# Kernel optimization log

Measured on AMD Instinct MI355X. Metric: run time of the kernel, lower is better.

Reference implementation:

```python
import jax, jax.numpy as jnp
import numpy as np

L = 2          # lags
D = 64         # latent_size
H = 128        # hidden_dim
NB = 3         # num_layers == n_blocks
B, T = 256, 1024


def setup_inputs() -> dict:
    key = jax.random.key(0)
    ks = jax.random.split(key, 20)
    sd = 0.1
    inp = {
        'x': jax.random.normal(ks[0], (B, T, D), jnp.float32),
        # f1: 3 hidden Linear(L*D=128 -> 128), all same shape so stacked, then out Linear(128 -> 64)
        'f1_hW': jax.random.normal(ks[1], (NB, H, H), jnp.float32) * sd,
        'f1_hb': jax.random.normal(ks[2], (NB, H), jnp.float32) * sd,
        'f1_oW': jax.random.normal(ks[3], (D, H), jnp.float32) * sd,
        'f1_ob': jax.random.normal(ks[4], (D,), jnp.float32) * sd,
        # flow: per block, s_net and t_net each Lin(D,H), Lin(H,H), Lin(H,D) (torch y = x@W.T + b)
        'sW0': jax.random.normal(ks[5], (NB, H, D), jnp.float32) * sd,
        'sb0': jax.random.normal(ks[6], (NB, H), jnp.float32) * sd,
        'sW1': jax.random.normal(ks[7], (NB, H, H), jnp.float32) * sd,
        'sb1': jax.random.normal(ks[8], (NB, H), jnp.float32) * sd,
        'sW2': jax.random.normal(ks[9], (NB, D, H), jnp.float32) * sd,
        'sb2': jax.random.normal(ks[10], (NB, D), jnp.float32) * sd,
        'tW0': jax.random.normal(ks[11], (NB, H, D), jnp.float32) * sd,
        'tb0': jax.random.normal(ks[12], (NB, H), jnp.float32) * sd,
        'tW1': jax.random.normal(ks[13], (NB, H, H), jnp.float32) * sd,
        'tb1': jax.random.normal(ks[14], (NB, H), jnp.float32) * sd,
        'tW2': jax.random.normal(ks[15], (NB, D, H), jnp.float32) * sd,
        'tb2': jax.random.normal(ks[16], (NB, D), jnp.float32) * sd,
    }
    return inp


def _leaky(z):
    return jnp.where(z >= 0, z, 0.2 * z)  # leap's NLayerLeakyMLP uses LeakyReLU(0.2)


def _flow(xt, sW0, sb0, sW1, sb1, sW2, sb2, tW0, tb0, tW1, tb1, tW2, tb2):
    # RealNVP-style affine coupling stack, no batch norm. xt: (N, D)
    m = (jnp.arange(D) % 2).astype(xt.dtype)  # alternating mask, flips per block
    u = xt
    logdet = jnp.zeros((xt.shape[0],), xt.dtype)
    for i in range(NB):
        mx = u * m
        s = jnp.tanh(mx @ sW0[i].T + sb0[i])
        s = jnp.tanh(s @ sW1[i].T + sb1[i])
        s = s @ sW2[i].T + sb2[i]
        t = jax.nn.relu(mx @ tW0[i].T + tb0[i])
        t = jax.nn.relu(t @ tW1[i].T + tb1[i])
        t = t @ tW2[i].T + tb2[i]
        u = mx + (1.0 - m) * (u - t) * jnp.exp(-s)
        logdet = logdet + jnp.sum(-(1.0 - m) * s, axis=1)
        m = 1.0 - m
    return u, logdet


def reference(x, f1_hW, f1_hb, f1_oW, f1_ob, sW0, sb0, sW1, sb1, sW2, sb2,
              tW0, tb0, tW1, tb1, tW2, tb2):
    Bs, Ts, Din = x.shape
    # f2 inverse flow on x[:, L:, :] flattened to (B*(T-L), D)
    xt = x[:, L:, :].reshape(-1, Din)
    x_inv, logdet = _flow(xt, sW0, sb0, sW1, sb1, sW2, sb2,
                          tW0, tb0, tW1, tb1, tW2, tb2)
    x_inv = x_inv.reshape(Bs, Ts - L, Din)
    # vectorized sliding-window MLP (replaces the per-timestep python loop)
    idx = jnp.arange(Ts - L)[:, None] + jnp.arange(L)        # (T-L, L)
    win = x[:, idx, :].reshape(Bs, Ts - L, L * Din)          # (B, T-L, L*D)
    h = win
    for i in range(NB):
        h = _leaky(h @ f1_hW[i].T + f1_hb[i])
    residuals = h @ f1_oW.T + f1_ob - x_inv                  # (B, T-L, D)
    log_abs_det_jacobian = jnp.sum(logdet.reshape(Bs, Ts - L), axis=1)  # (B,)
    return residuals, log_abs_det_jacobian
```

## Files before the change

kernel.cpp:

```cpp
#include <hip/hip_runtime.h>

#define DEV __device__ __forceinline__

typedef __attribute__((ext_vector_type(8)))  short bf16x8;
typedef __attribute__((ext_vector_type(4)))  short s16x4;
typedef __attribute__((ext_vector_type(4)))  float f32x4;
typedef __attribute__((ext_vector_type(16))) float f32x16;
typedef __attribute__((ext_vector_type(4)))  unsigned u32x4;

constexpr int Tt = 1024, TLr = 1022;
constexpr long WSW_BYTES = 704512;

#define MFMA32(a,b,c) __builtin_amdgcn_mfma_f32_32x32x16_bf16((a),(b),(c),0,0,0)

#define GLDS16(gp, lp) __builtin_amdgcn_global_load_lds( \
    (__attribute__((address_space(1))) void*)(void*)(gp), \
    (__attribute__((address_space(3))) void*)(void*)(lp), 16, 0, 0)

DEV short bf16hi(float f){
  unsigned u = __builtin_bit_cast(unsigned, f);
  u += 0x7FFFu + ((u >> 16) & 1u);
  return (short)(u >> 16);
}
DEV float bf2f(short h){
  unsigned u = ((unsigned)(unsigned short)h) << 16;
  return __builtin_bit_cast(float, u);
}
DEV void splitbf(float f, short &h, short &l){
  h = bf16hi(f);
  l = bf16hi(f - bf2f(h));
}

DEV unsigned cvtpk(float a, float b){
  unsigned r;
  asm("v_cvt_pk_bf16_f32 %0, %1, %2" : "=v"(r) : "v"(a), "v"(b));
  return r;
}
DEV void plswap(unsigned &a, unsigned &b){
  auto r = __builtin_amdgcn_permlane32_swap((int)a, (int)b, false, false);
  a = (unsigned)r[0]; b = (unsigned)r[1];
}

template<int A> DEV float actf(float x){
  if constexpr (A == 1){
    float e = __expf(2.f * x);
    return 1.f - 2.f * __builtin_amdgcn_rcpf(e + 1.f);
  } else if constexpr (A == 2){
    return fmaxf(x, 0.f);
  } else if constexpr (A == 3){
    return x >= 0.f ? x : 0.2f * x;
  }
  return x;
}

template<int BYTES>
DEV void pref(const char* __restrict__ wsW, long off, char* dst, int tid){
  #pragma unroll
  for (int it = 0; it < BYTES / 4096; ++it)
    GLDS16(wsW + off + it * 4096 + tid * 16, dst + it * 4096 + tid * 16);
}

DEV void packTile(const f32x16& c, unsigned (&Bg0)[4], unsigned (&Bg1)[4]){
  unsigned p0 = cvtpk(c[0], c[1]),  p1 = cvtpk(c[2], c[3]);
  unsigned p2 = cvtpk(c[4], c[5]),  p3 = cvtpk(c[6], c[7]);
  plswap(p0, p2); plswap(p1, p3);
  Bg0[0] = p0; Bg0[1] = p1; Bg0[2] = p2; Bg0[3] = p3;
  p0 = cvtpk(c[8],  c[9]);  p1 = cvtpk(c[10], c[11]);
  p2 = cvtpk(c[12], c[13]); p3 = cvtpk(c[14], c[15]);
  plswap(p0, p2); plswap(p1, p3);
  Bg1[0] = p0; Bg1[1] = p1; Bg1[2] = p2; Bg1[3] = p3;
}

template<int KT,int G,int GI,int MOUT,bool LO,int ACT,int MODE>
DEV void computeMT(const char* __restrict__ Ws, const float* __restrict__ bias,
                   const unsigned (&Bin)[2][8][4], unsigned (&Bout)[2][8][4],
                   f32x16 (&uA)[2][2], float (&ldet)[2],
                   float* __restrict__ residBase, int keep, int rowW,
                   int lane, int h4)
{
  constexpr int BS = LO ? 2048 : 1024;
  f32x16 acc[2];
  #pragma unroll
  for (int q = 0; q < 4; ++q){
    f32x4 bv = *(const f32x4*)(bias + 32 * MOUT + 8 * q + h4);
    #pragma unroll
    for (int j = 0; j < 4; ++j){ acc[0][4*q+j] = bv[j]; acc[1][4*q+j] = bv[j]; }
  }
  #pragma unroll
  for (int kt = 0; kt < KT; ++kt){
    const char* wp = Ws + (kt * G + GI) * BS + lane * 16;
    bf16x8 Ah = *(const bf16x8*)wp;
    #pragma unroll
    for (int n = 0; n < 2; ++n){
      u32x4 bw = {Bin[n][kt][0], Bin[n][kt][1], Bin[n][kt][2], Bin[n][kt][3]};
      acc[n] = MFMA32(Ah, __builtin_bit_cast(bf16x8, bw), acc[n]);
    }
    if constexpr (LO){
      bf16x8 Al = *(const bf16x8*)(wp + 1024);
      #pragma unroll
      for (int n = 0; n < 2; ++n){
        u32x4 bw = {Bin[n][kt][0], Bin[n][kt][1], Bin[n][kt][2], Bin[n][kt][3]};
        acc[n] = MFMA32(Al, __builtin_bit_cast(bf16x8, bw), acc[n]);
      }
    }
  }
  if constexpr (MODE == 0){
    #pragma unroll
    for (int n = 0; n < 2; ++n){
      #pragma unroll
      for (int i = 0; i < 16; ++i) acc[n][i] = actf<ACT>(acc[n][i]);
      packTile(acc[n], Bout[n][2 * MOUT], Bout[n][2 * MOUT + 1]);
    }
  } else if constexpr (MODE == 1){
    #pragma unroll
    for (int n = 0; n < 2; ++n)
      #pragma unroll
      for (int r = 0; r < 16; ++r)
        if ((r & 1) != keep) uA[MOUT][n][r] -= acc[n][r];
  } else if constexpr (MODE == 2){
    #pragma unroll
    for (int n = 0; n < 2; ++n)
      #pragma unroll
      for (int r = 0; r < 16; ++r)
        if ((r & 1) != keep){
          uA[MOUT][n][r] *= __expf(-acc[n][r]);
          ldet[n] -= acc[n][r];
        }
  } else {
    const int col = lane & 31;
    #pragma unroll
    for (int n = 0; n < 2; ++n){
      const int tau = rowW + n * 32 + col;
      if (tau < TLr){
        float* rp = residBase + (long)tau * 64 + 32 * MOUT + h4;
        #pragma unroll
        for (int q = 0; q < 4; ++q){
          f32x4 st;
          #pragma unroll
          for (int j = 0; j < 4; ++j)
            st[j] = acc[n][4 * q + j] - uA[MOUT][n][4 * q + j];
          *(f32x4*)(rp + 8 * q) = st;
        }
      }
    }
  }
}

DEV void buildMaskedB(const f32x16 (&u)[2][2], unsigned (&B)[2][8][4], int keep){
  const float mOdd  = (keep == 1) ? 1.f : 0.f;
  const float mEven = 1.f - mOdd;
  #pragma unroll
  for (int n = 0; n < 2; ++n)
    #pragma unroll
    for (int mi = 0; mi < 2; ++mi){
      f32x16 v;
      #pragma unroll
      for (int r = 0; r < 16; ++r)
        v[r] = u[mi][n][r] * ((r & 1) ? mOdd : mEven);
      packTile(v, B[n][2 * mi], B[n][2 * mi + 1]);
    }
}

DEV void buildWin(unsigned (&B)[2][8][4], const float* __restrict__ xb,
                  int rowW, int lane){
  const int col = lane & 31, h = lane >> 5;
  #pragma unroll
  for (int n = 0; n < 2; ++n){
    const int tau = rowW + n * 32 + col;
    #pragma unroll
    for (int g = 0; g < 8; ++g){
      int xr = tau + (g >= 4 ? 1 : 0);
      if (xr > Tt - 1) xr = Tt - 1;
      const int fo = (16 * g + 8 * h) & 63;
      const float* p = xb + xr * 64 + fo;
      f32x4 a = *(const f32x4*)p, b = *(const f32x4*)(p + 4);
      B[n][g][0] = cvtpk(a[0], a[1]); B[n][g][1] = cvtpk(a[2], a[3]);
      B[n][g][2] = cvtpk(b[0], b[1]); B[n][g][3] = cvtpk(b[2], b[3]);
    }
  }
}

__global__ void pnl_conv(const float* __restrict__ sW0, const float* __restrict__ sW1,
                         const float* __restrict__ sW2, const float* __restrict__ tW0,
                         const float* __restrict__ tW1, const float* __restrict__ tW2,
                         const float* __restrict__ f1_hW, const float* __restrict__ f1_oW,
                         char* __restrict__ wsW)
{
  const int cid = blockIdx.x * 256 + threadIdx.x;
  const float* src; long base; int hs, unit, BS, lg; bool LO;
  if (cid < 24576){
    const int blk = cid >> 13, r = cid & 8191;
    const long bb = (long)blk * 196608;
    if      (r < 1024){ src = tW0 + blk*8192;  hs=6; base=bb;        BS=1024; lg=2; LO=false; unit=r; }
    else if (r < 3072){ src = tW1 + blk*16384; hs=7; base=bb+16384;  BS=1024; lg=1; LO=false; unit=r-1024; }
    else if (r < 4096){ src = tW2 + blk*8192;  hs=7; base=bb+49152;  BS=1024; lg=1; LO=false; unit=r-3072; }
    else if (r < 5120){ src = sW0 + blk*8192;  hs=6; base=bb+65536;  BS=2048; lg=1; LO=true;  unit=r-4096; }
    else if (r < 7168){ src = sW1 + blk*16384; hs=7; base=bb+98304;  BS=2048; lg=0; LO=true;  unit=r-5120; }
    else              { src = sW2 + blk*8192;  hs=7; base=bb+163840; BS=2048; lg=0; LO=true;  unit=r-7168; }
  } else {
    const int r = cid - 24576;
    if (r < 6144){ const int l = r >> 11; src = f1_hW + l*16384; hs=7; base=589824+(long)l*32768; BS=1024; lg=1; LO=false; unit=r&2047; }
    else         { src = f1_oW; hs=7; base=688128; BS=1024; lg=1; LO=false; unit=r-6144; }
  }
  const int e    = unit << 3;
  const int feat = e >> hs;
  const int k    = e & ((1 << hs) - 1);
  const int m    = feat >> 5;
  const int stage = m >> lg;
  const int gi    = m & ((1 << lg) - 1);
  const int lane  = (feat & 31) | (((k >> 3) & 1) << 5);
  const long off  = base + (long)stage * 16384
                  + (long)((((k >> 4) << lg) + gi) * BS) + lane * 16;
  const float* sp = src + ((long)feat << hs) + k;
  f32x4 v0 = *(const f32x4*)sp, v1 = *(const f32x4*)(sp + 4);
  s16x4 ha, hb, la, lb;
  #pragma unroll
  for (int j = 0; j < 4; ++j){
    short hh, ll;
    splitbf(v0[j], hh, ll); ha[j] = hh; la[j] = ll;
    splitbf(v1[j], hh, ll); hb[j] = hh; lb[j] = ll;
  }
  *(s16x4*)(wsW + off)     = ha;
  *(s16x4*)(wsW + off + 8) = hb;
  if (LO){
    *(s16x4*)(wsW + off + 1024)     = la;
    *(s16x4*)(wsW + off + 1024 + 8) = lb;
  }
}

#define CMT(KT,G,GI,MOUT,LO,ACT,MODE,WS,BIAS,BIN,BOUT) \
  computeMT<KT,G,GI,MOUT,LO,ACT,MODE>(WS,BIAS,BIN,BOUT,uA,ldet,residBase,keep,rowW,lane,h4)

__global__ __launch_bounds__(256, 2)
void pnl_main(const float* __restrict__ x,
              const float* __restrict__ f1_hb, const float* __restrict__ f1_ob,
              const float* __restrict__ sb0, const float* __restrict__ sb1,
              const float* __restrict__ sb2, const float* __restrict__ tb0,
              const float* __restrict__ tb1, const float* __restrict__ tb2,
              const char* __restrict__ wsW,
              float* __restrict__ resid, float* __restrict__ wsPart)
{
  __shared__ __align__(16) char Wb[2][16384];

  const int tid  = threadIdx.x, w = tid >> 6, lane = tid & 63;
  const int col  = lane & 31, h4 = (lane >> 5) * 4;
  const int bIdx = blockIdx.x >> 2;
  const int t0w  = (blockIdx.x & 3) << 8;
  const int rowW = t0w + w * 64;
  const float* xb = x + (long)bIdx * Tt * 64;
  float* __restrict__ residBase = resid + (long)bIdx * TLr * 64;

  pref<16384>(wsW, 0, Wb[0], tid);

  f32x16 uA[2][2];
  #pragma unroll
  for (int mi = 0; mi < 2; ++mi)
    #pragma unroll
    for (int n = 0; n < 2; ++n){
      int xr = rowW + n * 32 + col + 2; if (xr > Tt - 1) xr = Tt - 1;
      #pragma unroll
      for (int q = 0; q < 4; ++q){
        f32x4 v = *(const f32x4*)(xb + xr * 64 + 32 * mi + 8 * q + h4);
        #pragma unroll
        for (int j = 0; j < 4; ++j) uA[mi][n][4 * q + j] = v[j];
      }
    }

  float ldet[2] = {0.f, 0.f};
  unsigned Bx[2][8][4], By[2][8][4];

  buildMaskedB(uA, Bx, 1);
  __syncthreads();

  #pragma unroll 1
  for (int blk = 0; blk < 3; ++blk){
    const long bb = (long)blk * 196608;
    const int keep = 1 - (blk & 1);
    const float* tb0b = tb0 + blk * 128; const float* tb1b = tb1 + blk * 128;
    const float* tb2b = tb2 + blk * 64;
    const float* sb0b = sb0 + blk * 128; const float* sb1b = sb1 + blk * 128;
    const float* sb2b = sb2 + blk * 64;

    pref<16384>(wsW, bb + 16384, Wb[1], tid);
    CMT(4,4,0,0,false,2,0, Wb[0], tb0b, Bx, By);
    CMT(4,4,1,1,false,2,0, Wb[0], tb0b, Bx, By);
    CMT(4,4,2,2,false,2,0, Wb[0], tb0b, Bx, By);
    CMT(4,4,3,3,false,2,0, Wb[0], tb0b, Bx, By);
    __syncthreads();
    pref<16384>(wsW, bb + 32768, Wb[0], tid);
    CMT(8,2,0,0,false,2,0, Wb[1], tb1b, By, Bx);
    CMT(8,2,1,1,false,2,0, Wb[1], tb1b, By, Bx);
    __syncthreads();
    pref<16384>(wsW, bb + 49152, Wb[1], tid);
    CMT(8,2,0,2,false,2,0, Wb[0], tb1b, By, Bx);
    CMT(8,2,1,3,false,2,0, Wb[0], tb1b, By, Bx);
    __syncthreads();
    pref<16384>(wsW, bb + 65536, Wb[0], tid);
    CMT(8,2,0,0,false,0,1, Wb[1], tb2b, Bx, By);
    CMT(8,2,1,1,false,0,1, Wb[1], tb2b, Bx, By);
    buildMaskedB(uA, By, keep);
    __syncthreads();
    pref<16384>(wsW, bb + 81920, Wb[1], tid);
    CMT(4,2,0,0,true,1,0, Wb[0], sb0b, By, Bx);
    CMT(4,2,1,1,true,1,0, Wb[0], sb0b, By, Bx);
    __syncthreads();
    pref<16384>(wsW, bb + 98304, Wb[0], tid);
    CMT(4,2,0,2,true,1,0, Wb[1], sb0b, By, Bx);
    CMT(4,2,1,3,true,1,0, Wb[1], sb0b, By, Bx);
    __syncthreads();
    pref<16384>(wsW, bb + 114688, Wb[1], tid);
    CMT(8,1,0,0,true,1,0, Wb[0], sb1b, Bx, By);
    __syncthreads();
    pref<16384>(wsW, bb + 131072, Wb[0], tid);
    CMT(8,1,0,1,true,1,0, Wb[1], sb1b, Bx, By);
    __syncthreads();
    pref<16384>(wsW, bb + 147456, Wb[1], tid);
    CMT(8,1,0,2,true,1,0, Wb[0], sb1b, Bx, By);
    __syncthreads();
    pref<16384>(wsW, bb + 163840, Wb[0], tid);
    CMT(8,1,0,3,true,1,0, Wb[1], sb1b, Bx, By);
    __syncthreads();
    pref<16384>(wsW, bb + 180224, Wb[1], tid);
    CMT(8,1,0,0,true,0,2, Wb[0], sb2b, By, Bx);
    __syncthreads();
    if (blk < 2) pref<16384>(wsW, bb + 196608, Wb[0], tid);
    else         pref<16384>(wsW, 589824,      Wb[0], tid);
    CMT(8,1,0,1,true,0,2, Wb[1], sb2b, By, Bx);
    if (blk < 2) buildMaskedB(uA, Bx, 1 - ((blk + 1) & 1));
    else         buildWin(Bx, xb, rowW, lane);
    __syncthreads();
  }

  {
    const int keep = 0;
    const float* tbD = f1_hb;
    (void)tbD;
    pref<16384>(wsW, 606208, Wb[1], tid);
    CMT(8,2,0,0,false,3,0, Wb[0], f1_hb, Bx, By);
    CMT(8,2,1,1,false,3,0, Wb[0], f1_hb, Bx, By);
    __syncthreads();
    pref<16384>(wsW, 622592, Wb[0], tid);
    CMT(8,2,0,2,false,3,0, Wb[1], f1_hb, Bx, By);
    CMT(8,2,1,3,false,3,0, Wb[1], f1_hb, Bx, By);
    __syncthreads();
    pref<16384>(wsW, 638976, Wb[1], tid);
    CMT(8,2,0,0,false,3,0, Wb[0], f1_hb + 128, By, Bx);
    CMT(8,2,1,1,false,3,0, Wb[0], f1_hb + 128, By, Bx);
    __syncthreads();
    pref<16384>(wsW, 655360, Wb[0], tid);
    CMT(8,2,0,2,false,3,0, Wb[1], f1_hb + 128, By, Bx);
    CMT(8,2,1,3,false,3,0, Wb[1], f1_hb + 128, By, Bx);
    __syncthreads();
    pref<16384>(wsW, 671744, Wb[1], tid);
    CMT(8,2,0,0,false,3,0, Wb[0], f1_hb + 256, Bx, By);
    CMT(8,2,1,1,false,3,0, Wb[0], f1_hb + 256, Bx, By);
    __syncthreads();
    pref<16384>(wsW, 688128, Wb[0], tid);
    CMT(8,2,0,2,false,3,0, Wb[1], f1_hb + 256, Bx, By);
    CMT(8,2,1,3,false,3,0, Wb[1], f1_hb + 256, Bx, By);
    __syncthreads();
    CMT(8,2,0,0,false,0,3, Wb[0], f1_ob, By, Bx);
    CMT(8,2,1,1,false,0,3, Wb[0], f1_ob, By, Bx);
  }

  const int tau0 = rowW + col, tau1 = rowW + 32 + col;
  float s = (tau0 < TLr ? ldet[0] : 0.f) + (tau1 < TLr ? ldet[1] : 0.f);
  #pragma unroll
  for (int off = 1; off < 64; off <<= 1) s += __shfl_xor(s, off);
  if (lane == 0) wsPart[blockIdx.x * 4 + w] = s;
}

__global__ void pnl_ldet(const float* __restrict__ ws, float* __restrict__ outLd){
  const int b = threadIdx.x;
  float s = 0.f;
  #pragma unroll
  for (int t = 0; t < 16; ++t) s += ws[b * 16 + t];
  outLd[b] = s;
}

extern "C" void kernel_launch(void* const* d_in, const int* in_sizes, int n_in,
                              void* d_out, int out_size, void* d_ws, size_t ws_size,
                              hipStream_t stream){
  const float* x     = (const float*)d_in[0];
  const float* f1_hW = (const float*)d_in[1];
  const float* f1_hb = (const float*)d_in[2];
  const float* f1_oW = (const float*)d_in[3];
  const float* f1_ob = (const float*)d_in[4];
  const float* sW0   = (const float*)d_in[5];
  const float* sb0   = (const float*)d_in[6];
  const float* sW1   = (const float*)d_in[7];
  const float* sb1   = (const float*)d_in[8];
  const float* sW2   = (const float*)d_in[9];
  const float* sb2   = (const float*)d_in[10];
  const float* tW0   = (const float*)d_in[11];
  const float* tb0   = (const float*)d_in[12];
  const float* tW1   = (const float*)d_in[13];
  const float* tb1   = (const float*)d_in[14];
  const float* tW2   = (const float*)d_in[15];
  const float* tb2   = (const float*)d_in[16];

  char*  wsW    = (char*)d_ws;
  float* wsPart = (float*)(wsW + WSW_BYTES);
  float* resid  = (float*)d_out;
  float* outLd  = resid + (long)256 * TLr * 64;

  pnl_conv<<<dim3(124), dim3(256), 0, stream>>>(sW0, sW1, sW2, tW0, tW1, tW2,
                                                f1_hW, f1_oW, wsW);
  pnl_main<<<dim3(1024), dim3(256), 0, stream>>>(
      x, f1_hb, f1_ob, sb0, sb1, sb2, tb0, tb1, tb2, wsW, resid, wsPart);
  pnl_ldet<<<dim3(1), dim3(256), 0, stream>>>(wsPart, outLd);
}
```

Baseline: 232.3 us.

## Triple-buffer weight stages in LDS with vmcnt-based waits and single barriers

Result: slower. 248.3 us (+6.9%).

```diff
diff --git a/kernel.cpp b/kernel.cpp
--- a/kernel.cpp
+++ b/kernel.cpp
@@ -16,6 +16,11 @@
 #define GLDS16(gp, lp) __builtin_amdgcn_global_load_lds( \
     (__attribute__((address_space(1))) void*)(void*)(gp), \
     (__attribute__((address_space(3))) void*)(void*)(lp), 16, 0, 0)
+
+#define WAITV4() asm volatile("s_waitcnt vmcnt(4)" ::: "memory")
+#define WAITV0() asm volatile("s_waitcnt vmcnt(0)" ::: "memory")
+#define BARX()   do { __builtin_amdgcn_s_barrier(); \
+                      __builtin_amdgcn_sched_barrier(0); } while(0)
 
 DEV short bf16hi(float f){
   unsigned u = __builtin_bit_cast(unsigned, f);
@@ -53,11 +58,11 @@
   return x;
 }
 
-template<int BYTES>
-DEV void pref(const char* __restrict__ wsW, long off, char* dst, int tid){
-  #pragma unroll
-  for (int it = 0; it < BYTES / 4096; ++it)
-    GLDS16(wsW + off + it * 4096 + tid * 16, dst + it * 4096 + tid * 16);
+DEV void prefStage(const char* __restrict__ wsW, long k, char* dst, int tid){
+  const char* s = wsW + (k << 14);
+  #pragma unroll
+  for (int it = 0; it < 4; ++it)
+    GLDS16(s + it * 4096 + tid * 16, dst + it * 4096 + tid * 16);
 }
 
 DEV void packTile(const f32x16& c, unsigned (&Bg0)[4], unsigned (&Bg1)[4]){
@@ -240,7 +245,10 @@
               const char* __restrict__ wsW,
               float* __restrict__ resid, float* __restrict__ wsPart)
 {
-  __shared__ __align__(16) char Wb[2][16384];
+  __shared__ __align__(16) char Wb[49152];
+  char* const W0 = Wb;
+  char* const W1 = Wb + 16384;
+  char* const W2 = Wb + 32768;
 
   const int tid  = threadIdx.x, w = tid >> 6, lane = tid & 63;
   const int col  = lane & 31, h4 = (lane >> 5) * 4;
@@ -250,8 +258,6 @@
   const float* xb = x + (long)bIdx * Tt * 64;
   float* __restrict__ residBase = resid + (long)bIdx * TLr * 64;
 
-  pref<16384>(wsW, 0, Wb[0], tid);
-
   f32x16 uA[2][2];
   #pragma unroll
   for (int mi = 0; mi < 2; ++mi)
@@ -265,102 +271,85 @@
         for (int j = 0; j < 4; ++j) uA[mi][n][4 * q + j] = v[j];
       }
     }
+  __builtin_amdgcn_sched_barrier(0);
+
+  prefStage(wsW, 0, W0, tid);
+  prefStage(wsW, 1, W1, tid);
 
   float ldet[2] = {0.f, 0.f};
   unsigned Bx[2][8][4], By[2][8][4];
 
   buildMaskedB(uA, Bx, 1);
-  __syncthreads();
 
   #pragma unroll 1
   for (int blk = 0; blk < 3; ++blk){
-    const long bb = (long)blk * 196608;
+    const long kb = (long)blk * 12;
     const int keep = 1 - (blk & 1);
     const float* tb0b = tb0 + blk * 128; const float* tb1b = tb1 + blk * 128;
     const float* tb2b = tb2 + blk * 64;
     const float* sb0b = sb0 + blk * 128; const float* sb1b = sb1 + blk * 128;
     const float* sb2b = sb2 + blk * 64;
 
-    pref<16384>(wsW, bb + 16384, Wb[1], tid);
-    CMT(4,4,0,0,false,2,0, Wb[0], tb0b, Bx, By);
-    CMT(4,4,1,1,false,2,0, Wb[0], tb0b, Bx, By);
-    CMT(4,4,2,2,false,2,0, Wb[0], tb0b, Bx, By);
-    CMT(4,4,3,3,false,2,0, Wb[0], tb0b, Bx, By);
-    __syncthreads();
-    pref<16384>(wsW, bb + 32768, Wb[0], tid);
-    CMT(8,2,0,0,false,2,0, Wb[1], tb1b, By, Bx);
-    CMT(8,2,1,1,false,2,0, Wb[1], tb1b, By, Bx);
-    __syncthreads();
-    pref<16384>(wsW, bb + 49152, Wb[1], tid);
-    CMT(8,2,0,2,false,2,0, Wb[0], tb1b, By, Bx);
-    CMT(8,2,1,3,false,2,0, Wb[0], tb1b, By, Bx);
-    __syncthreads();
-    pref<16384>(wsW, bb + 65536, Wb[0], tid);
-    CMT(8,2,0,0,false,0,1, Wb[1], tb2b, Bx, By);
-    CMT(8,2,1,1,false,0,1, Wb[1], tb2b, Bx, By);
+    WAITV4(); BARX(); prefStage(wsW, kb + 2, W2, tid);
+    CMT(4,4,0,0,false,2,0, W0, tb0b, Bx, By);
+    CMT(4,4,1,1,false,2,0, W0, tb0b, Bx, By);
+    CMT(4,4,2,2,false,2,0, W0, tb0b, Bx, By);
+    CMT(4,4,3,3,false,2,0, W0, tb0b, Bx, By);
+    WAITV4(); BARX(); prefStage(wsW, kb + 3, W0, tid);
+    CMT(8,2,0,0,false,2,0, W1, tb1b, By, Bx);
+    CMT(8,2,1,1,false,2,0, W1, tb1b, By, Bx);
+    WAITV4(); BARX(); prefStage(wsW, kb + 4, W1, tid);
+    CMT(8,2,0,2,false,2,0, W2, tb1b, By, Bx);
+    CMT(8,2,1,3,false,2,0, W2, tb1b, By, Bx);
+    WAITV4(); BARX(); prefStage(wsW, kb + 5, W2, tid);
+    CMT(8,2,0,0,false,0,1, W0, tb2b, Bx, By);
+    CMT(8,2,1,1,false,0,1, W0, tb2b, Bx, By);
     buildMaskedB(uA, By, keep);
-    __syncthreads();
-    pref<16384>(wsW, bb + 81920, Wb[1], tid);
-    CMT(4,2,0,0,true,1,0, Wb[0], sb0b, By, Bx);
-    CMT(4,2,1,1,true,1,0, Wb[0], sb0b, By, Bx);
-    __syncthreads();
-    pref<16384>(wsW, bb + 98304, Wb[0], tid);
-    CMT(4,2,0,2,true,1,0, Wb[1], sb0b, By, Bx);
-    CMT(4,2,1,3,true,1,0, Wb[1], sb0b, By, Bx);
-    __syncthreads();
-    pref<16384>(wsW, bb + 114688, Wb[1], tid);
-    CMT(8,1,0,0,true,1,0, Wb[0], sb1b, Bx, By);
-    __syncthreads();
-    pref<16384>(wsW, bb + 131072, Wb[0], tid);
-    CMT(8,1,0,1,true,1,0, Wb[1], sb1b, Bx, By);
-    __syncthreads();
-    pref<16384>(wsW, bb + 147456, Wb[1], tid);
-    CMT(8,1,0,2,true,1,0, Wb[0], sb1b, Bx, By);
-    __syncthreads();
-    pref<16384>(wsW, bb + 163840, Wb[0], tid);
-    CMT(8,1,0,3,true,1,0, Wb[1], sb1b, Bx, By);
-    __syncthreads();
-    pref<16384>(wsW, bb + 180224, Wb[1], tid);
-    CMT(8,1,0,0,true,0,2, Wb[0], sb2b, By, Bx);
-    __syncthreads();
-    if (blk < 2) pref<16384>(wsW, bb + 196608, Wb[0], tid);
-    else         pref<16384>(wsW, 589824,      Wb[0], tid);
-    CMT(8,1,0,1,true,0,2, Wb[1], sb2b, By, Bx);
+    WAITV4(); BARX(); prefStage(wsW, kb + 6, W0, tid);
+    CMT(4,2,0,0,true,1,0, W1, sb0b, By, Bx);
+    CMT(4,2,1,1,true,1,0, W1, sb0b, By, Bx);
+    WAITV4(); BARX(); prefStage(wsW, kb + 7, W1, tid);
+    CMT(4,2,0,2,true,1,0, W2, sb0b, By, Bx);
+    CMT(4,2,1,3,true,1,0, W2, sb0b, By, Bx);
+    WAITV4(); BARX(); prefStage(wsW, kb + 8, W2, tid);
+    CMT(8,1,0,0,true,1,0, W0, sb1b, Bx, By);
+    WAITV4(); BARX(); prefStage(wsW, kb + 9, W0, tid);
+    CMT(8,1,0,1,true,1,0, W1, sb1b, Bx, By);
+    WAITV4(); BARX(); prefStage(wsW, kb + 10, W1, tid);
+    CMT(8,1,0,2,true,1,0, W2, sb1b, Bx, By);
+    WAITV4(); BARX(); prefStage(wsW, kb + 11, W2, tid);
+    CMT(8,1,0,3,true,1,0, W0, sb1b, Bx, By);
+    WAITV4(); BARX(); prefStage(wsW, kb + 12, W0, tid);
+    CMT(8,1,0,0,true,0,2, W1, sb2b, By, Bx);
+    WAITV4(); BARX(); prefStage(wsW, kb + 13, W1, tid);
+    CMT(8,1,0,1,true,0,2, W2, sb2b, By, Bx);
     if (blk < 2) buildMaskedB(uA, Bx, 1 - ((blk + 1) & 1));
     else         buildWin(Bx, xb, rowW, lane);
-    __syncthreads();
   }
 
   {
     const int keep = 0;
-    const float* tbD = f1_hb;
-    (void)tbD;
-    pref<16384>(wsW, 606208, Wb[1], tid);
-    CMT(8,2,0,0,false,3,0, Wb[0], f1_hb, Bx, By);
-    CMT(8,2,1,1,false,3,0, Wb[0], f1_hb, Bx, By);
-    __syncthreads();
-    pref<16384>(wsW, 622592, Wb[0], tid);
-    CMT(8,2,0,2,false,3,0, Wb[1], f1_hb, Bx, By);
-    CMT(8,2,1,3,false,3,0, Wb[1], f1_hb, Bx, By);
-    __syncthreads();
-    pref<16384>(wsW, 638976, Wb[1], tid);
-    CMT(8,2,0,0,false,3,0, Wb[0], f1_hb + 128, By, Bx);
-    CMT(8,2,1,1,false,3,0, Wb[0], f1_hb + 128, By, Bx);
-    __syncthreads();
-    pref<16384>(wsW, 655360, Wb[0], tid);
-    CMT(8,2,0,2,false,3,0, Wb[1], f1_hb + 128, By, Bx);
-    CMT(8,2,1,3,false,3,0, Wb[1], f1_hb + 128, By, Bx);
-    __syncthreads();
-    pref<16384>(wsW, 671744, Wb[1], tid);
-    CMT(8,2,0,0,false,3,0, Wb[0], f1_hb + 256, Bx, By);
-    CMT(8,2,1,1,false,3,0, Wb[0], f1_hb + 256, Bx, By);
-    __syncthreads();
-    pref<16384>(wsW, 688128, Wb[0], tid);
-    CMT(8,2,0,2,false,3,0, Wb[1], f1_hb + 256, Bx, By);
-    CMT(8,2,1,3,false,3,0, Wb[1], f1_hb + 256, Bx, By);
-    __syncthreads();
-    CMT(8,2,0,0,false,0,3, Wb[0], f1_ob, By, Bx);
-    CMT(8,2,1,1,false,0,3, Wb[0], f1_ob, By, Bx);
+    WAITV4(); BARX(); prefStage(wsW, 38, W2, tid);
+    CMT(8,2,0,0,false,3,0, W0, f1_hb, Bx, By);
+    CMT(8,2,1,1,false,3,0, W0, f1_hb, Bx, By);
+    WAITV4(); BARX(); prefStage(wsW, 39, W0, tid);
+    CMT(8,2,0,2,false,3,0, W1, f1_hb, Bx, By);
+    CMT(8,2,1,3,false,3,0, W1, f1_hb, Bx, By);
+    WAITV4(); BARX(); prefStage(wsW, 40, W1, tid);
+    CMT(8,2,0,0,false,3,0, W2, f1_hb + 128, By, Bx);
+    CMT(8,2,1,1,false,3,0, W2, f1_hb + 128, By, Bx);
+    WAITV4(); BARX(); prefStage(wsW, 41, W2, tid);
+    CMT(8,2,0,2,false,3,0, W0, f1_hb + 128, By, Bx);
+    CMT(8,2,1,3,false,3,0, W0, f1_hb + 128, By, Bx);
+    WAITV4(); BARX(); prefStage(wsW, 42, W0, tid);
+    CMT(8,2,0,0,false,3,0, W1, f1_hb + 256, Bx, By);
+    CMT(8,2,1,1,false,3,0, W1, f1_hb + 256, Bx, By);
+    WAITV4(); BARX();
+    CMT(8,2,0,2,false,3,0, W2, f1_hb + 256, Bx, By);
+    CMT(8,2,1,3,false,3,0, W2, f1_hb + 256, Bx, By);
+    WAITV0(); BARX();
+    CMT(8,2,0,0,false,0,3, W0, f1_ob, By, Bx);
+    CMT(8,2,1,1,false,0,3, W0, f1_ob, By, Bx);
   }
 
   const int tau0 = rowW + col, tau1 = rowW + 32 + col;
```

## Drop bf16 hi/lo split for s-net first two layers and add MFMA priority

Applied to the files above, without the earlier changes.

Result: faster. 199.8 us, median of 2 (-14.0%).

```diff
diff --git a/kernel.cpp b/kernel.cpp
--- a/kernel.cpp
+++ b/kernel.cpp
@@ -9,7 +9,7 @@
 typedef __attribute__((ext_vector_type(4)))  unsigned u32x4;
 
 constexpr int Tt = 1024, TLr = 1022;
-constexpr long WSW_BYTES = 704512;
+constexpr long WSW_BYTES = 557056;
 
 #define MFMA32(a,b,c) __builtin_amdgcn_mfma_f32_32x32x16_bf16((a),(b),(c),0,0,0)
 
@@ -53,11 +53,11 @@
   return x;
 }
 
-template<int BYTES>
-DEV void pref(const char* __restrict__ wsW, long off, char* dst, int tid){
-  #pragma unroll
-  for (int it = 0; it < BYTES / 4096; ++it)
-    GLDS16(wsW + off + it * 4096 + tid * 16, dst + it * 4096 + tid * 16);
+DEV void prefStage(const char* __restrict__ wsW, long k, char* dst, int tid){
+  const char* s = wsW + (k << 14);
+  #pragma unroll
+  for (int it = 0; it < 4; ++it)
+    GLDS16(s + it * 4096 + tid * 16, dst + it * 4096 + tid * 16);
 }
 
 DEV void packTile(const f32x16& c, unsigned (&Bg0)[4], unsigned (&Bg1)[4]){
@@ -86,6 +86,7 @@
     #pragma unroll
     for (int j = 0; j < 4; ++j){ acc[0][4*q+j] = bv[j]; acc[1][4*q+j] = bv[j]; }
   }
+  __builtin_amdgcn_s_setprio(1);
   #pragma unroll
   for (int kt = 0; kt < KT; ++kt){
     const char* wp = Ws + (kt * G + GI) * BS + lane * 16;
@@ -104,6 +105,7 @@
       }
     }
   }
+  __builtin_amdgcn_s_setprio(0);
   if constexpr (MODE == 0){
     #pragma unroll
     for (int n = 0; n < 2; ++n){
@@ -190,17 +192,17 @@
   const float* src; long base; int hs, unit, BS, lg; bool LO;
   if (cid < 24576){
     const int blk = cid >> 13, r = cid & 8191;
-    const long bb = (long)blk * 196608;
+    const long bb = (long)blk * 147456;
     if      (r < 1024){ src = tW0 + blk*8192;  hs=6; base=bb;        BS=1024; lg=2; LO=false; unit=r; }
     else if (r < 3072){ src = tW1 + blk*16384; hs=7; base=bb+16384;  BS=1024; lg=1; LO=false; unit=r-1024; }
     else if (r < 4096){ src = tW2 + blk*8192;  hs=7; base=bb+49152;  BS=1024; lg=1; LO=false; unit=r-3072; }
-    else if (r < 5120){ src = sW0 + blk*8192;  hs=6; base=bb+65536;  BS=2048; lg=1; LO=true;  unit=r-4096; }
-    else if (r < 7168){ src = sW1 + blk*16384; hs=7; base=bb+98304;  BS=2048; lg=0; LO=true;  unit=r-5120; }
-    else              { src = sW2 + blk*8192;  hs=7; base=bb+163840; BS=2048; lg=0; LO=true;  unit=r-7168; }
+    else if (r < 5120){ src = sW0 + blk*8192;  hs=6; base=bb+65536;  BS=1024; lg=2; LO=false; unit=r-4096; }
+    else if (r < 7168){ src = sW1 + blk*16384; hs=7; base=bb+81920;  BS=1024; lg=1; LO=false; unit=r-5120; }
+    else              { src = sW2 + blk*8192;  hs=7; base=bb+114688; BS=2048; lg=0; LO=true;  unit=r-7168; }
   } else {
     const int r = cid - 24576;
-    if (r < 6144){ const int l = r >> 11; src = f1_hW + l*16384; hs=7; base=589824+(long)l*32768; BS=1024; lg=1; LO=false; unit=r&2047; }
-    else         { src = f1_oW; hs=7; base=688128; BS=1024; lg=1; LO=false; unit=r-6144; }
+    if (r < 6144){ const int l = r >> 11; src = f1_hW + l*16384; hs=7; base=442368+(long)l*32768; BS=1024; lg=1; LO=false; unit=r&2047; }
+    else         { src = f1_oW; hs=7; base=540672; BS=1024; lg=1; LO=false; unit=r-6144; }
   }
   const int e    = unit << 3;
   const int feat = e >> hs;
@@ -250,7 +252,7 @@
   const float* xb = x + (long)bIdx * Tt * 64;
   float* __restrict__ residBase = resid + (long)bIdx * TLr * 64;
 
-  pref<16384>(wsW, 0, Wb[0], tid);
+  prefStage(wsW, 0, Wb[0], tid);
 
   f32x16 uA[2][2];
   #pragma unroll
@@ -274,58 +276,54 @@
 
   #pragma unroll 1
   for (int blk = 0; blk < 3; ++blk){
-    const long bb = (long)blk * 196608;
+    const int kb = blk * 9;
+    const int par = kb & 1;
+    char* const WA = Wb[par];
+    char* const WB = Wb[par ^ 1];
     const int keep = 1 - (blk & 1);
     const float* tb0b = tb0 + blk * 128; const float* tb1b = tb1 + blk * 128;
     const float* tb2b = tb2 + blk * 64;
     const float* sb0b = sb0 + blk * 128; const float* sb1b = sb1 + blk * 128;
     const float* sb2b = sb2 + blk * 64;
 
-    pref<16384>(wsW, bb + 16384, Wb[1], tid);
-    CMT(4,4,0,0,false,2,0, Wb[0], tb0b, Bx, By);
-    CMT(4,4,1,1,false,2,0, Wb[0], tb0b, Bx, By);
-    CMT(4,4,2,2,false,2,0, Wb[0], tb0b, Bx, By);
-    CMT(4,4,3,3,false,2,0, Wb[0], tb0b, Bx, By);
-    __syncthreads();
-    pref<16384>(wsW, bb + 32768, Wb[0], tid);
-    CMT(8,2,0,0,false,2,0, Wb[1], tb1b, By, Bx);
-    CMT(8,2,1,1,false,2,0, Wb[1], tb1b, By, Bx);
-    __syncthreads();
-    pref<16384>(wsW, bb + 49152, Wb[1], tid);
-    CMT(8,2,0,2,false,2,0, Wb[0], tb1b, By, Bx);
-    CMT(8,2,1,3,false,2,0, Wb[0], tb1b, By, Bx);
-    __syncthreads();
-    pref<16384>(wsW, bb + 65536, Wb[0], tid);
-    CMT(8,2,0,0,false,0,1, Wb[1], tb2b, Bx, By);
-    CMT(8,2,1,1,false,0,1, Wb[1], tb2b, Bx, By);
+    prefStage(wsW, kb + 1, WB, tid);
+    CMT(4,4,0,0,false,2,0, WA, tb0b, Bx, By);
+    CMT(4,4,1,1,false,2,0, WA, tb0b, Bx, By);
+    CMT(4,4,2,2,false,2,0, WA, tb0b, Bx, By);
+    CMT(4,4,3,3,false,2,0, WA, tb0b, Bx, By);
+    __syncthreads();
+    prefStage(wsW, kb + 2, WA, tid);
+    CMT(8,2,0,0,false,2,0, WB, tb1b, By, Bx);
+    CMT(8,2,1,1,false,2,0, WB, tb1b, By, Bx);
+    __syncthreads();
+    prefStage(wsW, kb + 3, WB, tid);
+    CMT(8,2,0,2,false,2,0, WA, tb1b, By, Bx);
+    CMT(8,2,1,3,false,2,0, WA, tb1b, By, Bx);
+    __syncthreads();
+    prefStage(wsW, kb + 4, WA, tid);
+    CMT(8,2,0,0,false,0,1, WB, tb2b, Bx, By);
+    CMT(8,2,1,1,false,0,1, WB, tb2b, Bx, By);
     buildMaskedB(uA, By, keep);
     __syncthreads();
-    pref<16384>(wsW, bb + 81920, Wb[1], tid);
-    CMT(4,2,0,0,true,1,0, Wb[0], sb0b, By, Bx);
-    CMT(4,2,1,1,true,1,0, Wb[0], sb0b, By, Bx);
-    __syncthreads();
-    pref<16384>(wsW, bb + 98304, Wb[0], tid);
-    CMT(4,2,0,2,true,1,0, Wb[1], sb0b, By, Bx);
-    CMT(4,2,1,3,true,1,0, Wb[1], sb0b, By, Bx);
-    __syncthreads();
-    pref<16384>(wsW, bb + 114688, Wb[1], tid);
-    CMT(8,1,0,0,true,1,0, Wb[0], sb1b, Bx, By);
-    __syncthreads();
-    pref<16384>(wsW, bb + 131072, Wb[0], tid);
-    CMT(8,1,0,1,true,1,0, Wb[1], sb1b, Bx, By);
-    __syncthreads();
-    pref<16384>(wsW, bb + 147456, Wb[1], tid);
-    CMT(8,1,0,2,true,1,0, Wb[0], sb1b, Bx, By);
-    __syncthreads();
-    pref<16384>(wsW, bb + 163840, Wb[0], tid);
-    CMT(8,1,0,3,true,1,0, Wb[1], sb1b, Bx, By);
-    __syncthreads();
-    pref<16384>(wsW, bb + 180224, Wb[1], tid);
-    CMT(8,1,0,0,true,0,2, Wb[0], sb2b, By, Bx);
-    __syncthreads();
-    if (blk < 2) pref<16384>(wsW, bb + 196608, Wb[0], tid);
-    else         pref<16384>(wsW, 589824,      Wb[0], tid);
-    CMT(8,1,0,1,true,0,2, Wb[1], sb2b, By, Bx);
+    prefStage(wsW, kb + 5, WB, tid);
+    CMT(4,4,0,0,false,1,0, WA, sb0b, By, Bx);
+    CMT(4,4,1,1,false,1,0, WA, sb0b, By, Bx);
+    CMT(4,4,2,2,false,1,0, WA, sb0b, By, Bx);
+    CMT(4,4,3,3,false,1,0, WA, sb0b, By, Bx);
+    __syncthreads();
+    prefStage(wsW, kb + 6, WA, tid);
+    CMT(8,2,0,0,false,1,0, WB, sb1b, Bx, By);
+    CMT(8,2,1,1,false,1,0, WB, sb1b, Bx, By);
+    __syncthreads();
+    prefStage(wsW, kb + 7, WB, tid);
+    CMT(8,2,0,2,false,1,0, WA, sb1b, Bx, By);
+    CMT(8,2,1,3,false,1,0, WA, sb1b, Bx, By);
+    __syncthreads();
+    prefStage(wsW, kb + 8, WA, tid);
+    CMT(8,1,0,0,true,0,2, WB, sb2b, By, Bx);
+    __syncthreads();
+    prefStage(wsW, kb + 9, WB, tid);
+    CMT(8,1,0,1,true,0,2, WA, sb2b, By, Bx);
     if (blk < 2) buildMaskedB(uA, Bx, 1 - ((blk + 1) & 1));
     else         buildWin(Bx, xb, rowW, lane);
     __syncthreads();
@@ -333,34 +331,34 @@
 
   {
     const int keep = 0;
-    const float* tbD = f1_hb;
-    (void)tbD;
-    pref<16384>(wsW, 606208, Wb[1], tid);
-    CMT(8,2,0,0,false,3,0, Wb[0], f1_hb, Bx, By);
-    CMT(8,2,1,1,false,3,0, Wb[0], f1_hb, Bx, By);
-    __syncthreads();
-    pref<16384>(wsW, 622592, Wb[0], tid);
-    CMT(8,2,0,2,false,3,0, Wb[1], f1_hb, Bx, By);
-    CMT(8,2,1,3,false,3,0, Wb[1], f1_hb, Bx, By);
-    __syncthreads();
-    pref<16384>(wsW, 638976, Wb[1], tid);
-    CMT(8,2,0,0,false,3,0, Wb[0], f1_hb + 128, By, Bx);
-    CMT(8,2,1,1,false,3,0, Wb[0], f1_hb + 128, By, Bx);
-    __syncthreads();
-    pref<16384>(wsW, 655360, Wb[0], tid);
-    CMT(8,2,0,2,false,3,0, Wb[1], f1_hb + 128, By, Bx);
-    CMT(8,2,1,3,false,3,0, Wb[1], f1_hb + 128, By, Bx);
-    __syncthreads();
-    pref<16384>(wsW, 671744, Wb[1], tid);
-    CMT(8,2,0,0,false,3,0, Wb[0], f1_hb + 256, Bx, By);
-    CMT(8,2,1,1,false,3,0, Wb[0], f1_hb + 256, Bx, By);
-    __syncthreads();
-    pref<16384>(wsW, 688128, Wb[0], tid);
-    CMT(8,2,0,2,false,3,0, Wb[1], f1_hb + 256, Bx, By);
-    CMT(8,2,1,3,false,3,0, Wb[1], f1_hb + 256, Bx, By);
-    __syncthreads();
-    CMT(8,2,0,0,false,0,3, Wb[0], f1_ob, By, Bx);
-    CMT(8,2,1,1,false,0,3, Wb[0], f1_ob, By, Bx);
+    char* const F1 = Wb[1];
+    char* const F0 = Wb[0];
+    prefStage(wsW, 28, F0, tid);
+    CMT(8,2,0,0,false,3,0, F1, f1_hb, Bx, By);
+    CMT(8,2,1,1,false,3,0, F1, f1_hb, Bx, By);
+    __syncthreads();
+    prefStage(wsW, 29, F1, tid);
+    CMT(8,2,0,2,false,3,0, F0, f1_hb, Bx, By);
+    CMT(8,2,1,3,false,3,0, F0, f1_hb, Bx, By);
+    __syncthreads();
+    prefStage(wsW, 30, F0, tid);
+    CMT(8,2,0,0,false,3,0, F1, f1_hb + 128, By, Bx);
+    CMT(8,2,1,1,false,3,0, F1, f1_hb + 128, By, Bx);
+    __syncthreads();
+    prefStage(wsW, 31, F1, tid);
+    CMT(8,2,0,2,false,3,0, F0, f1_hb + 128, By, Bx);
+    CMT(8,2,1,3,false,3,0, F0, f1_hb + 128, By, Bx);
+    __syncthreads();
+    prefStage(wsW, 32, F0, tid);
+    CMT(8,2,0,0,false,3,0, F1, f1_hb + 256, Bx, By);
+    CMT(8,2,1,1,false,3,0, F1, f1_hb + 256, Bx, By);
+    __syncthreads();
+    prefStage(wsW, 33, F1, tid);
+    CMT(8,2,0,2,false,3,0, F0, f1_hb + 256, Bx, By);
+    CMT(8,2,1,3,false,3,0, F0, f1_hb + 256, Bx, By);
+    __syncthreads();
+    CMT(8,2,0,0,false,0,3, F1, f1_ob, By, Bx);
+    CMT(8,2,1,1,false,0,3, F1, f1_ob, By, Bx);
   }
 
   const int tau0 = rowW + col, tau1 = rowW + 32 + col;
```
